# Kernel optimization log

Measured on AMD Instinct MI355X. Metric: run time of the kernel, lower is better.

Reference implementation:

```python
import jax, jax.numpy as jnp
import numpy as np

BS, L, D, H, NL, ITEM_NUM = 128, 64, 512, 8, 2, 100000
NEG_INF = -10000.0


def _ln(x):
    m = jnp.mean(x, axis=-1, keepdims=True)
    v = jnp.var(x, axis=-1, keepdims=True)
    return (x - m) * jax.lax.rsqrt(v + 1e-5)


def _user_encoder(input_embs, log_mask, pos_emb, qkv_w, out_w, ffn_w1, ffn_w2):
    # SASRec-style causal transformer encoder (post-LN blocks)
    B, S, d = input_embs.shape
    dh = d // H
    x = _ln(input_embs + pos_emb[None, :, :])
    pad = (log_mask != 0)                                  # [B,S]
    causal = jnp.tril(jnp.ones((S, S), dtype=bool))
    attn_ok = causal[None, :, :] & pad[:, None, :]         # [B,S,S]
    bias = jnp.where(attn_ok, 0.0, NEG_INF)[:, None, :, :]  # [B,1,S,S]
    for l in range(NL):
        qkv = x @ qkv_w[l]                                 # [B,S,3d]
        q, k, v = jnp.split(qkv, 3, axis=-1)
        q = q.reshape(B, S, H, dh).transpose(0, 2, 1, 3)
        k = k.reshape(B, S, H, dh).transpose(0, 2, 1, 3)
        v = v.reshape(B, S, H, dh).transpose(0, 2, 1, 3)
        scores = jnp.einsum('bhqd,bhkd->bhqk', q, k) / jnp.sqrt(jnp.asarray(dh, x.dtype)) + bias
        attn = jax.nn.softmax(scores, axis=-1)
        o = jnp.einsum('bhqk,bhkd->bhqd', attn, v).transpose(0, 2, 1, 3).reshape(B, S, d)
        x = _ln(x + o @ out_w[l])
        h = jax.nn.gelu(x @ ffn_w1[l])
        x = _ln(x + h @ ffn_w2[l])
    return x


def setup_inputs() -> dict:
    key = jax.random.key(0)
    ks = jax.random.split(key, 9)
    sample_items_id = jax.random.randint(ks[0], (BS, L + 1), 0, ITEM_NUM + 1)
    log_mask = jax.random.randint(ks[1], (BS, L), 0, 2).astype(jnp.float32)
    emb_table = (jax.random.normal(ks[2], (ITEM_NUM + 1, D), jnp.float32) * 0.02).at[0].set(0.0)
    pos_emb = jax.random.normal(ks[3], (L, D), jnp.float32) * 0.02
    qkv_w = jax.random.normal(ks[4], (NL, D, 3 * D), jnp.float32) * (D ** -0.5)
    out_w = jax.random.normal(ks[5], (NL, D, D), jnp.float32) * (D ** -0.5)
    ffn_w1 = jax.random.normal(ks[6], (NL, D, 4 * D), jnp.float32) * (D ** -0.5)
    ffn_w2 = jax.random.normal(ks[7], (NL, 4 * D, D), jnp.float32) * ((4 * D) ** -0.5)
    pop_prob = jax.random.uniform(ks[8], (ITEM_NUM + 1,), jnp.float32, 1e-6, 1.0)
    return dict(sample_items_id=sample_items_id, log_mask=log_mask, emb_table=emb_table,
                pos_emb=pos_emb, qkv_w=qkv_w, out_w=out_w, ffn_w1=ffn_w1, ffn_w2=ffn_w2,
                pop_prob=pop_prob)


def reference(sample_items_id, log_mask, emb_table, pos_emb, qkv_w, out_w, ffn_w1, ffn_w2, pop_prob):
    bs, l = log_mask.shape
    N = bs * (l + 1)
    items_flat = sample_items_id.reshape(-1)                        # [N]
    debias = jnp.log(pop_prob[items_flat])                          # [N]
    score_embs = emb_table[items_flat]                              # [N, D]
    input_embs = score_embs.reshape(bs, l + 1, -1)
    prec = _user_encoder(input_embs[:, :-1, :], log_mask, pos_emb, qkv_w, out_w, ffn_w1, ffn_w2)
    prec = prec.reshape(bs * l, -1)                                 # [bs*L, D]
    logits = prec @ score_embs.T - debias[None, :]                  # [bs*L, N]
    # padding-column mask (concat(log_mask, ones) == 0)
    pad_cols = jnp.concatenate([log_mask, jnp.ones((bs, 1), log_mask.dtype)], axis=1).reshape(-1) == 0
    logits = jnp.where(pad_cols[None, :], NEG_INF, logits)
    logits = logits.reshape(bs, l, N)
    # in-batch dedup mask: column k masked for batch i if item k appears in batch i's items
    id_list = sample_items_id.reshape(bs, l + 1)
    member = (items_flat[None, :, None] == id_list[:, None, :]).any(-1)   # [bs, N]
    target_col = jnp.arange(bs)[:, None] * (l + 1) + jnp.arange(1, l + 1)[None, :]  # [bs, L]
    is_target = jnp.arange(N)[None, None, :] == target_col[:, :, None]    # [bs, L, N]
    dedup = member[:, None, :] & ~is_target
    logits = jnp.where(dedup, NEG_INF, logits).reshape(bs * l, N)
    labels = target_col.reshape(-1)                                 # [bs*L]
    logp = jax.nn.log_softmax(logits, axis=-1)
    nll = -jnp.take_along_axis(logp, labels[:, None], axis=1)[:, 0]
    valid = (log_mask.reshape(-1) != 0).astype(logits.dtype)
    return (nll * valid).sum() / valid.sum()
```

## Files before the change

### kernel.cpp

```cpp
#include <hip/hip_runtime.h>
#include <hip/hip_bf16.h>
#include <cstdint>
#include <cstddef>

#define NEG_INF -10000.0f

constexpr int BSZ  = 128;
constexpr int SEQ  = 64;
constexpr int DIM  = 512;
constexpr int HEADS = 8;
constexpr int NLAYER = 2;
constexpr int NCOL = BSZ * (SEQ + 1);
constexpr int NCOLP = 8448;
constexpr int NROW = BSZ * SEQ;
constexpr int NSTRIP = NCOLP / 64;
constexpr float CMAX = 40.0f;

typedef __attribute__((ext_vector_type(8))) short bf16x8;
typedef __attribute__((ext_vector_type(4))) float f32x4;

__device__ __forceinline__ void async_copy16(const void* g, void* l) {
    __builtin_amdgcn_global_load_lds(
        (const __attribute__((address_space(1))) void*)g,
        (__attribute__((address_space(3))) void*)l, 16, 0, 0);
}

__device__ __forceinline__ float b2f(uint16_t u) {
    return __builtin_bit_cast(float, (uint32_t)u << 16);
}
__device__ __forceinline__ uint16_t f2b(float f) {
    __hip_bfloat16 h = __float2bfloat16(f);
    return __builtin_bit_cast(uint16_t, h);
}

__device__ __forceinline__ float gelu_f(float v) {
    float u = 0.7978845608028654f * (v + 0.044715f * v * v * v);
    return 0.5f * v * (1.0f + tanhf(u));
}

__device__ __forceinline__ void swizzle_rc(int id, int& ry, int& cx) {
    ry = (id & 7) * 8 + ((id >> 3) & 7);
    cx = id >> 6;
}

#define BAR() __builtin_amdgcn_s_barrier()
#define LGKM0() asm volatile("s_waitcnt lgkmcnt(0)" ::: "memory")
#define VMCNT(n) asm volatile("s_waitcnt vmcnt(" #n ")" ::: "memory")

__global__ __launch_bounds__(256) void gather_posln_kernel(
    const int* __restrict__ ids, const float* __restrict__ table,
    const float* __restrict__ pop, const float* __restrict__ pos,
    __hip_bfloat16* __restrict__ sebf, float* __restrict__ debias,
    __hip_bfloat16* __restrict__ xb) {
    const int w = threadIdx.x >> 6, lane = threadIdx.x & 63;
    const int k = blockIdx.x * 4 + w;
    const int b = k / 65, s = k - b * 65;
    const int id = ids[k];
    const float* src = table + (size_t)id * DIM + lane * 8;
    float4 u0 = *(const float4*)src;
    float4 u1 = *(const float4*)(src + 4);
    float v[8] = {u0.x, u0.y, u0.z, u0.w, u1.x, u1.y, u1.z, u1.w};
    bf16x8 se;
    #pragma unroll
    for (int j = 0; j < 8; j++) se[j] = (short)f2b(v[j]);
    *(bf16x8*)((uint16_t*)sebf + (size_t)k * DIM + lane * 8) = se;
    if (lane == 0) debias[k] = logf(pop[id]);
    if (s < 64) {
        const float* pp = pos + (size_t)s * DIM + lane * 8;
        float4 p0 = *(const float4*)pp;
        float4 p1 = *(const float4*)(pp + 4);
        float t[8] = {v[0] + p0.x, v[1] + p0.y, v[2] + p0.z, v[3] + p0.w,
                      v[4] + p1.x, v[5] + p1.y, v[6] + p1.z, v[7] + p1.w};
        float sum = 0.f, sq = 0.f;
        #pragma unroll
        for (int j = 0; j < 8; j++) { sum += t[j]; sq += t[j] * t[j]; }
        #pragma unroll
        for (int off = 32; off > 0; off >>= 1) {
            sum += __shfl_xor(sum, off, 64);
            sq  += __shfl_xor(sq,  off, 64);
        }
        const float mean = sum * (1.0f / 512.0f);
        const float var  = sq * (1.0f / 512.0f) - mean * mean;
        const float rs = rsqrtf(var + 1e-5f);
        bf16x8 o;
        #pragma unroll
        for (int j = 0; j < 8; j++) o[j] = (short)f2b((t[j] - mean) * rs);
        *(bf16x8*)((uint16_t*)xb + (size_t)(b * 64 + s) * DIM + lane * 8) = o;
    }
}

__global__ __launch_bounds__(256) void mask_kernel(
    const int* __restrict__ ids, const float* __restrict__ log_mask,
    uint8_t* __restrict__ colmask, uint8_t* __restrict__ padcol) {
    const int bi = blockIdx.x >> 3, seg = blockIdx.x & 7;
    __shared__ int sid[65];
    if (threadIdx.x < 65) sid[threadIdx.x] = ids[bi * 65 + threadIdx.x];
    __syncthreads();
    const int kend = (seg + 1) * (NCOLP / 8);
    for (int k = seg * (NCOLP / 8) + threadIdx.x; k < kend; k += 256) {
        uint8_t cmv, pcv;
        if (k < NCOL) {
            const int id = ids[k];
            bool mem = false;
            #pragma unroll
            for (int j = 0; j < 65; j++) mem |= (sid[j] == id);
            const int i2 = k / 65, jj = k - i2 * 65;
            const bool pc = (jj < 64) && (log_mask[i2 * 64 + jj] == 0.0f);
            cmv = (mem || pc) ? 1 : 0;
            pcv = pc ? 1 : 0;
        } else { cmv = 1; pcv = 1; }
        colmask[(size_t)bi * NCOLP + k] = cmv;
        if (bi == 0) padcol[k] = pcv;
    }
}

__global__ __launch_bounds__(256) void transpose_bf16_kernel(
    const float* __restrict__ W, __hip_bfloat16* __restrict__ WT, int K, int N) {
    __shared__ float tile[32][33];
    const size_t loff = (size_t)blockIdx.z * K * N;
    const int nt = blockIdx.x * 32, kt = blockIdx.y * 32;
    const int c = threadIdx.x & 31, r = threadIdx.x >> 5;
    #pragma unroll
    for (int p = 0; p < 4; p++)
        tile[p * 8 + r][c] = W[loff + (size_t)(kt + p * 8 + r) * N + nt + c];
    __syncthreads();
    #pragma unroll
    for (int p = 0; p < 4; p++)
        WT[loff + (size_t)(nt + p * 8 + r) * K + kt + c] = __float2bfloat16(tile[c][p * 8 + r]);
}

__global__ __launch_bounds__(256) void resid_ln_kernel(
    __hip_bfloat16* __restrict__ xb, const __hip_bfloat16* __restrict__ y) {
    const int w = threadIdx.x >> 6, lane = threadIdx.x & 63;
    const int row = blockIdx.x * 4 + w;
    uint16_t* xp = (uint16_t*)xb + (size_t)row * DIM + lane * 8;
    const uint16_t* yp = (const uint16_t*)y + (size_t)row * DIM + lane * 8;
    bf16x8 xv = *(const bf16x8*)xp;
    bf16x8 yv = *(const bf16x8*)yp;
    float t[8];
    float sum = 0.f, sq = 0.f;
    #pragma unroll
    for (int j = 0; j < 8; j++) {
        t[j] = b2f((uint16_t)xv[j]) + b2f((uint16_t)yv[j]);
        sum += t[j]; sq += t[j] * t[j];
    }
    #pragma unroll
    for (int off = 32; off > 0; off >>= 1) {
        sum += __shfl_xor(sum, off, 64);
        sq  += __shfl_xor(sq,  off, 64);
    }
    const float mean = sum * (1.0f / 512.0f);
    const float var  = sq * (1.0f / 512.0f) - mean * mean;
    const float rs = rsqrtf(var + 1e-5f);
    bf16x8 o;
    #pragma unroll
    for (int j = 0; j < 8; j++) o[j] = (short)f2b((t[j] - mean) * rs);
    *(bf16x8*)xp = o;
}

template<int TN, bool GELU>
__global__ __launch_bounds__(256) void gemm_bt_kernel(
    const __hip_bfloat16* __restrict__ A, const __hip_bfloat16* __restrict__ Bt,
    __hip_bfloat16* __restrict__ C, int N, int K) {
    __shared__ uint16_t As[2][128][32];
    __shared__ uint16_t Bs[2][TN][32];
    const int tid = threadIdx.x, w = tid >> 6, lane = tid & 63;
    const int quad = lane >> 4, l15 = lane & 15;
    constexpr int AI = (TN == 128) ? 4 : 2;
    const int wr = (TN == 128) ? (w >> 1) : w;
    const int wc = (TN == 128) ? (w & 1) : 0;
    const int rowbase = wr * (AI * 16);
    int ry, cx;
    swizzle_rc(blockIdx.x, ry, cx);
    const int row0 = ry * 128, col0 = cx * TN;
    const uint16_t* Ag = (const uint16_t*)A;
    const uint16_t* Bg = (const uint16_t*)Bt;
    const int sr = lane >> 2, sc = (lane & 3) * 8;
    f32x4 acc[AI][4];
    #pragma unroll
    for (int i = 0; i < AI; i++)
        #pragma unroll
        for (int j = 0; j < 4; j++) acc[i][j] = {0.f, 0.f, 0.f, 0.f};

    for (int k0 = 0; k0 < K; k0 += 64) {
        #pragma unroll
        for (int h = 0; h < 2; h++) {
            #pragma unroll
            for (int i = 0; i < 2; i++) {
                const int rb = w * 32 + i * 16;
                async_copy16(Ag + (size_t)(row0 + rb + sr) * K + k0 + h * 32 + sc, &As[h][rb][0]);
            }
            if (TN == 128) {
                #pragma unroll
                for (int i = 0; i < 2; i++) {
                    const int rb = w * 32 + i * 16;
                    async_copy16(Bg + (size_t)(col0 + rb + sr) * K + k0 + h * 32 + sc, &Bs[h][rb][0]);
                }
            } else {
                const int rb = w * 16;
                async_copy16(Bg + (size_t)(col0 + rb + sr) * K + k0 + h * 32 + sc, &Bs[h][rb][0]);
            }
        }
        __syncthreads();
        #pragma unroll
        for (int h = 0; h < 2; h++) {
            bf16x8 af[AI], bfr[4];
            #pragma unroll
            for (int i = 0; i < AI; i++)
                af[i] = *(const bf16x8*)&As[h][rowbase + i * 16 + l15][quad * 8];
            #pragma unroll
            for (int j = 0; j < 4; j++)
                bfr[j] = *(const bf16x8*)&Bs[h][wc * 64 + j * 16 + l15][quad * 8];
            #pragma unroll
            for (int i = 0; i < AI; i++)
                #pragma unroll
                for (int j = 0; j < 4; j++)
                    acc[i][j] = __builtin_amdgcn_mfma_f32_16x16x32_bf16(af[i], bfr[j], acc[i][j], 0, 0, 0);
        }
        __syncthreads();
    }
    #pragma unroll
    for (int i = 0; i < AI; i++) {
        #pragma unroll
        for (int r = 0; r < 4; r++) {
            const int row = row0 + rowbase + i * 16 + quad * 4 + r;
            #pragma unroll
            for (int j = 0; j < 4; j++) {
                const int col = col0 + wc * 64 + j * 16 + l15;
                float v = acc[i][j][r];
                if (GELU) v = gelu_f(v);
                C[(size_t)row * N + col] = __float2bfloat16(v);
            }
        }
    }
}

__global__ __launch_bounds__(256) void attn_mfma_kernel(
    const __hip_bfloat16* __restrict__ qkv, const float* __restrict__ log_mask,
    __hip_bfloat16* __restrict__ obuf) {
    constexpr int QS = 72;
    constexpr int VS32 = 36;
    __shared__ uint16_t Qs[64 * QS];
    __shared__ uint16_t Ks_[64 * QS];
    __shared__ uint16_t Ps[64 * QS];
    __shared__ uint32_t Vt32[64 * VS32];
    __shared__ float mask_s[64];
    const int b = blockIdx.x >> 3, h = blockIdx.x & 7;
    const int tid = threadIdx.x, w = tid >> 6, lane = tid & 63;
    const int quad = lane >> 4, l15 = lane & 15;
    const uint16_t* qg = (const uint16_t*)qkv;

    if (tid < 64) mask_s[tid] = log_mask[b * 64 + tid];
    #pragma unroll
    for (int it = 0; it < 2; it++) {
        const int idx = it * 256 + tid;
        const int s = idx >> 3, c = (idx & 7) * 8;
        const size_t gbase = (size_t)(b * 64 + s) * 1536 + h * 64 + c;
        *(bf16x8*)&Qs[s * QS + c]  = *(const bf16x8*)&qg[gbase];
        *(bf16x8*)&Ks_[s * QS + c] = *(const bf16x8*)&qg[gbase + 512];
    }
    {
        const int sp = tid >> 3;
        const int c = (tid & 7) * 8;
        const size_t gbase = (size_t)(b * 64 + sp * 2) * 1536 + 1024 + h * 64 + c;
        bf16x8 v0 = *(const bf16x8*)&qg[gbase];
        bf16x8 v1 = *(const bf16x8*)&qg[gbase + 1536];
        #pragma unroll
        for (int jj = 0; jj < 8; jj++)
            Vt32[(c + jj) * VS32 + sp] =
                (uint32_t)(uint16_t)v0[jj] | ((uint32_t)(uint16_t)v1[jj] << 16);
    }
    __syncthreads();

    f32x4 sacc[4];
    #pragma unroll
    for (int j = 0; j < 4; j++) sacc[j] = {0.f, 0.f, 0.f, 0.f};
    #pragma unroll
    for (int k0 = 0; k0 < 2; k0++) {
        bf16x8 aq = *(const bf16x8*)&Qs[(w * 16 + l15) * QS + k0 * 32 + quad * 8];
        #pragma unroll
        for (int j = 0; j < 4; j++) {
            bf16x8 bk = *(const bf16x8*)&Ks_[(j * 16 + l15) * QS + k0 * 32 + quad * 8];
            sacc[j] = __builtin_amdgcn_mfma_f32_16x16x32_bf16(aq, bk, sacc[j], 0, 0, 0);
        }
    }
    #pragma unroll
    for (int r = 0; r < 4; r++) {
        const int q = w * 16 + quad * 4 + r;
        float vals[4];
        float vmax = -3.0e38f;
        #pragma unroll
        for (int j = 0; j < 4; j++) {
            const int col = j * 16 + l15;
            const bool ok = (col <= q) && (mask_s[col] != 0.0f);
            float v = sacc[j][r] * 0.125f + (ok ? 0.0f : NEG_INF);
            vals[j] = v;
            vmax = fmaxf(vmax, v);
        }
        #pragma unroll
        for (int off = 1; off < 16; off <<= 1) vmax = fmaxf(vmax, __shfl_xor(vmax, off, 64));
        float e[4], s = 0.f;
        #pragma unroll
        for (int j = 0; j < 4; j++) { e[j] = __expf(vals[j] - vmax); s += e[j]; }
        #pragma unroll
        for (int off = 1; off < 16; off <<= 1) s += __shfl_xor(s, off, 64);
        const float inv = 1.0f / s;
        #pragma unroll
        for (int j = 0; j < 4; j++)
            Ps[q * QS + j * 16 + l15] = f2b(e[j] * inv);
    }
    __syncthreads();

    f32x4 oacc[4];
    #pragma unroll
    for (int j = 0; j < 4; j++) oacc[j] = {0.f, 0.f, 0.f, 0.f};
    #pragma unroll
    for (int k0 = 0; k0 < 2; k0++) {
        bf16x8 ap = *(const bf16x8*)&Ps[(w * 16 + l15) * QS + k0 * 32 + quad * 8];
        #pragma unroll
        for (int j = 0; j < 4; j++) {
            bf16x8 bv = *(const bf16x8*)&Vt32[(j * 16 + l15) * VS32 + k0 * 16 + quad * 4];
            oacc[j] = __builtin_amdgcn_mfma_f32_16x16x32_bf16(ap, bv, oacc[j], 0, 0, 0);
        }
    }
    #pragma unroll
    for (int r = 0; r < 4; r++) {
        const int q = w * 16 + quad * 4 + r;
        #pragma unroll
        for (int j = 0; j < 4; j++) {
            const int d = j * 16 + l15;
            obuf[(size_t)(b * 64 + q) * 512 + h * 64 + d] = __float2bfloat16(oacc[j][r]);
        }
    }
}

template<int EPI>
__global__ __launch_bounds__(512) void gemm256_kernel(
    const __hip_bfloat16* __restrict__ A, const __hip_bfloat16* __restrict__ Bt,
    __hip_bfloat16* __restrict__ C, int N, int K,
    const float* __restrict__ debias, const uint8_t* __restrict__ colmask,
    float* __restrict__ partials) {
    __shared__ uint16_t SA[2][2][128 * 64];
    __shared__ uint16_t SB[2][2][128 * 64];
    __shared__ float dc_s[256];
    __shared__ uint8_t cm_s[4][256];

    const int tid = threadIdx.x;
    const int w = tid >> 6, lane = tid & 63;
    const int quad = lane >> 4, l15 = lane & 15;
    const int wr = w >> 2, wc = w & 3;

    const int kb = blockIdx.x >> 3;
    const int ry = (blockIdx.x & 7) * 4 + (kb & 3), cx = kb >> 2;
    const int row0 = ry * 256, col0 = cx * 256;

    const uint16_t* Ag = (const uint16_t*)A;
    const uint16_t* Bg = (const uint16_t*)Bt;

    if (EPI == 2) {
        if (tid < 256) dc_s[tid] = debias[col0 + tid] + CMAX;
        #pragma unroll
        for (int j = 0; j < 2; j++) {
            const int e = j * 512 + tid;
            cm_s[e >> 8][e & 255] =
                colmask[(size_t)((row0 >> 6) + (e >> 8)) * NCOLP + col0 + (e & 255)];
        }
    }

    const int tb0 = w << 6, tb1 = 512 + (w << 6);
    const uint16_t* gA[2][2];
    const uint16_t* gB[2][2];
    #pragma unroll
    for (int j = 0; j < 2; j++) {
        const int t = j * 512 + (w << 6) + lane;
        const int r = t >> 3;
        const int s = (t & 7) ^ (r & 7);
        #pragma unroll
        for (int h = 0; h < 2; h++) {
            gA[h][j] = Ag + (size_t)(row0 + h * 128 + r) * K + s * 8;
            gB[h][j] = Bg + (size_t)(col0 + h * 128 + r) * K + s * 8;
        }
    }

    #define STAGE_A(tile, half, k0) do { \
        async_copy16(gA[half][0] + (k0), &SA[tile][half][tb0 * 8]); \
        async_copy16(gA[half][1] + (k0), &SA[tile][half][tb1 * 8]); } while (0)
    #define STAGE_B(tile, half, k0) do { \
        async_copy16(gB[half][0] + (k0), &SB[tile][half][tb0 * 8]); \
        async_copy16(gB[half][1] + (k0), &SB[tile][half][tb1 * 8]); } while (0)

    auto fragA = [&](int tile, int m, int kk) -> bf16x8 {
        return *(const bf16x8*)&SA[tile][wr]
            [((m * 16 + l15) << 6) + ((((kk << 2) + quad) ^ (l15 & 7)) << 3)];
    };
    auto fragB = [&](int tile, int n, int kk) -> bf16x8 {
        return *(const bf16x8*)&SB[tile][wc >> 1]
            [(((wc & 1) * 64 + n * 16 + l15) << 6) + ((((kk << 2) + quad) ^ (l15 & 7)) << 3)];
    };

    f32x4 acc[8][4];
    #pragma unroll
    for (int m = 0; m < 8; m++)
        #pragma unroll
        for (int n = 0; n < 4; n++) acc[m][n] = {0.f, 0.f, 0.f, 0.f};

    STAGE_A(0, 0, 0); STAGE_A(0, 1, 0);
    STAGE_B(0, 0, 0); STAGE_B(0, 1, 0);
    STAGE_A(1, 0, 64); STAGE_B(1, 0, 64);
    VMCNT(4);
    BAR();

    const int niters = K >> 7;
    bf16x8 af[4][2], bA[2][2], bB[2][2];
    for (int it = 0; it < niters; ++it) {
        const bool st = (it + 1 < niters);
        const int kc = it << 7;
        const int kn = kc + 128;

        #pragma unroll
        for (int m = 0; m < 4; m++) { af[m][0] = fragA(0, m, 0); af[m][1] = fragA(0, m, 1); }
        #pragma unroll
        for (int n = 0; n < 2; n++) { bA[n][0] = fragB(0, n, 0); bA[n][1] = fragB(0, n, 1); }
        STAGE_A(1, 1, kc + 64);
        BAR(); LGKM0();
        __builtin_amdgcn_s_setprio(1);
        #pragma unroll
        for (int m = 0; m < 4; m++)
            #pragma unroll
            for (int n = 0; n < 2; n++) {
                acc[m][n] = __builtin_amdgcn_mfma_f32_16x16x32_bf16(af[m][0], bA[n][0], acc[m][n], 0, 0, 0);
                acc[m][n] = __builtin_amdgcn_mfma_f32_16x16x32_bf16(af[m][1], bA[n][1], acc[m][n], 0, 0, 0);
            }
        __builtin_amdgcn_s_setprio(0);
        BAR();

        #pragma unroll
        for (int n = 0; n < 2; n++) { bB[n][0] = fragB(0, n + 2, 0); bB[n][1] = fragB(0, n + 2, 1); }
        STAGE_B(1, 1, kc + 64);
        BAR(); LGKM0();
        __builtin_amdgcn_s_setprio(1);
        #pragma unroll
        for (int m = 0; m < 4; m++)
            #pragma unroll
            for (int n = 0; n < 2; n++) {
                acc[m][n + 2] = __builtin_amdgcn_mfma_f32_16x16x32_bf16(af[m][0], bB[n][0], acc[m][n + 2], 0, 0, 0);
                acc[m][n + 2] = __builtin_amdgcn_mfma_f32_16x16x32_bf16(af[m][1], bB[n][1], acc[m][n + 2], 0, 0, 0);
            }
        __builtin_amdgcn_s_setprio(0);
        BAR();

        #pragma unroll
        for (int m = 0; m < 4; m++) { af[m][0] = fragA(0, m + 4, 0); af[m][1] = fragA(0, m + 4, 1); }
        if (st) STAGE_B(0, 0, kn);
        BAR(); LGKM0();
        __builtin_amdgcn_s_setprio(1);
        #pragma unroll
        for (int m = 0; m < 4; m++)
            #pragma unroll
            for (int n = 0; n < 2; n++) {
                acc[m + 4][n + 2] = __builtin_amdgcn_mfma_f32_16x16x32_bf16(af[m][0], bB[n][0], acc[m + 4][n + 2], 0, 0, 0);
                acc[m + 4][n + 2] = __builtin_amdgcn_mfma_f32_16x16x32_bf16(af[m][1], bB[n][1], acc[m + 4][n + 2], 0, 0, 0);
            }
        __builtin_amdgcn_s_setprio(0);
        BAR();

        if (st) STAGE_A(0, 0, kn);
        __builtin_amdgcn_s_setprio(1);
        #pragma unroll
        for (int m = 0; m < 4; m++)
            #pragma unroll
            for (int n = 0; n < 2; n++) {
                acc[m + 4][n] = __builtin_amdgcn_mfma_f32_16x16x32_bf16(af[m][0], bA[n][0], acc[m + 4][n], 0, 0, 0);
                acc[m + 4][n] = __builtin_amdgcn_mfma_f32_16x16x32_bf16(af[m][1], bA[n][1], acc[m + 4][n], 0, 0, 0);
            }
        __builtin_amdgcn_s_setprio(0);
        if (st) { VMCNT(4); } else { VMCNT(0); }
        BAR();

        #pragma unroll
        for (int m = 0; m < 4; m++) { af[m][0] = fragA(1, m, 0); af[m][1] = fragA(1, m, 1); }
        #pragma unroll
        for (int n = 0; n < 2; n++) { bA[n][0] = fragB(1, n, 0); bA[n][1] = fragB(1, n, 1); }
        if (st) STAGE_A(0, 1, kn);
        BAR(); LGKM0();
        __builtin_amdgcn_s_setprio(1);
        #pragma unroll
        for (int m = 0; m < 4; m++)
            #pragma unroll
            for (int n = 0; n < 2; n++) {
                acc[m][n] = __builtin_amdgcn_mfma_f32_16x16x32_bf16(af[m][0], bA[n][0], acc[m][n], 0, 0, 0);
                acc[m][n] = __builtin_amdgcn_mfma_f32_16x16x32_bf16(af[m][1], bA[n][1], acc[m][n], 0, 0, 0);
            }
        __builtin_amdgcn_s_setprio(0);
        BAR();

        #pragma unroll
        for (int n = 0; n < 2; n++) { bB[n][0] = fragB(1, n + 2, 0); bB[n][1] = fragB(1, n + 2, 1); }
        if (st) STAGE_B(0, 1, kn);
        BAR(); LGKM0();
        __builtin_amdgcn_s_setprio(1);
        #pragma unroll
        for (int m = 0; m < 4; m++)
            #pragma unroll
            for (int n = 0; n < 2; n++) {
                acc[m][n + 2] = __builtin_amdgcn_mfma_f32_16x16x32_bf16(af[m][0], bB[n][0], acc[m][n + 2], 0, 0, 0);
                acc[m][n + 2] = __builtin_amdgcn_mfma_f32_16x16x32_bf16(af[m][1], bB[n][1], acc[m][n + 2], 0, 0, 0);
            }
        __builtin_amdgcn_s_setprio(0);
        BAR();

        #pragma unroll
        for (int m = 0; m < 4; m++) { af[m][0] = fragA(1, m + 4, 0); af[m][1] = fragA(1, m + 4, 1); }
        if (st) STAGE_B(1, 0, kn + 64);
        BAR(); LGKM0();
        __builtin_amdgcn_s_setprio(1);
        #pragma unroll
        for (int m = 0; m < 4; m++)
            #pragma unroll
            for (int n = 0; n < 2; n++) {
                acc[m + 4][n + 2] = __builtin_amdgcn_mfma_f32_16x16x32_bf16(af[m][0], bB[n][0], acc[m + 4][n + 2], 0, 0, 0);
                acc[m + 4][n + 2] = __builtin_amdgcn_mfma_f32_16x16x32_bf16(af[m][1], bB[n][1], acc[m + 4][n + 2], 0, 0, 0);
            }
        __builtin_amdgcn_s_setprio(0);
        BAR();

        if (st) STAGE_A(1, 0, kn + 64);
        __builtin_amdgcn_s_setprio(1);
        #pragma unroll
        for (int m = 0; m < 4; m++)
            #pragma unroll
            for (int n = 0; n < 2; n++) {
                acc[m + 4][n] = __builtin_amdgcn_mfma_f32_16x16x32_bf16(af[m][0], bA[n][0], acc[m + 4][n], 0, 0, 0);
                acc[m + 4][n] = __builtin_amdgcn_mfma_f32_16x16x32_bf16(af[m][1], bA[n][1], acc[m + 4][n], 0, 0, 0);
            }
        __builtin_amdgcn_s_setprio(0);
        if (st) { VMCNT(4); BAR(); }
    }

    if (EPI == 2) {
        const int strip = cx * 4 + wc;
        #pragma unroll
        for (int m = 0; m < 8; m++) {
            #pragma unroll
            for (int r = 0; r < 4; r++) {
                const int lrow = wr * 128 + m * 16 + quad * 4 + r;
                const int row = row0 + lrow;
                float s = 0.f;
                #pragma unroll
                for (int n = 0; n < 4; n++) {
                    const int lcol = wc * 64 + n * 16 + l15;
                    float t = acc[m][n][r] - dc_s[lcol];
                    t = (cm_s[lrow >> 6][lcol] != 0) ? -1.0e30f : t;
                    s += __expf(t);
                }
                #pragma unroll
                for (int off = 1; off < 16; off <<= 1) s += __shfl_xor(s, off, 64);
                if (l15 == 0) partials[(size_t)row * NSTRIP + strip] = s;
            }
        }
    } else {
        #pragma unroll
        for (int m = 0; m < 8; m++) {
            #pragma unroll
            for (int r = 0; r < 4; r++) {
                const int row = row0 + wr * 128 + m * 16 + quad * 4 + r;
                #pragma unroll
                for (int n = 0; n < 4; n++) {
                    const int col = col0 + wc * 64 + n * 16 + l15;
                    float v = acc[m][n][r];
                    if (EPI == 1) v = gelu_f(v);
                    C[(size_t)row * N + col] = __float2bfloat16(v);
                }
            }
        }
    }
    #undef STAGE_A
    #undef STAGE_B
}

__global__ __launch_bounds__(256) void label_kernel(
    const __hip_bfloat16* __restrict__ xb, const __hip_bfloat16* __restrict__ sebf,
    const float* __restrict__ debias, const uint8_t* __restrict__ padcol,
    float* __restrict__ lab) {
    const int w = threadIdx.x >> 6, lane = threadIdx.x & 63;
    const int row = blockIdx.x * 4 + w;
    const int b = row >> 6, s0 = row & 63;
    const int k = b * 65 + s0 + 1;
    const uint16_t* xp = (const uint16_t*)xb + (size_t)row * DIM + lane * 8;
    const uint16_t* sp = (const uint16_t*)sebf + (size_t)k * DIM + lane * 8;
    bf16x8 xv = *(const bf16x8*)xp;
    bf16x8 sv = *(const bf16x8*)sp;
    float a = 0.f;
    #pragma unroll
    for (int j = 0; j < 8; j++) a += b2f((uint16_t)xv[j]) * b2f((uint16_t)sv[j]);
    #pragma unroll
    for (int off = 32; off > 0; off >>= 1) a += __shfl_xor(a, off, 64);
    if (lane == 0)
        lab[row] = padcol[k] ? NEG_INF : (a - debias[k]);
}

__global__ __launch_bounds__(256) void combine_kernel(
    const float* __restrict__ partials, const float* __restrict__ label_logit,
    const float* __restrict__ log_mask, float* __restrict__ bsums) {
    const int row = blockIdx.x * 256 + threadIdx.x;
    const float lab = label_logit[row];
    float Ls = __expf(lab - CMAX);
    const float4* pr = (const float4*)(partials + (size_t)row * NSTRIP);
    for (int t = 0; t < NSTRIP / 4; t++) {
        float4 v = pr[t];
        Ls += v.x + v.y + v.z + v.w;
    }
    const float lse = CMAX + logf(Ls);
    const float valid = (log_mask[row] != 0.0f) ? 1.0f : 0.0f;
    float a = (lse - lab) * valid;
    float c = valid;
    __shared__ float sa[4], sc_[4];
    #pragma unroll
    for (int off = 32; off > 0; off >>= 1) {
        a += __shfl_down(a, off, 64);
        c += __shfl_down(c, off, 64);
    }
    const int lane = threadIdx.x & 63, w = threadIdx.x >> 6;
    if (lane == 0) { sa[w] = a; sc_[w] = c; }
    __syncthreads();
    if (threadIdx.x == 0) {
        bsums[blockIdx.x * 2 + 0] = sa[0] + sa[1] + sa[2] + sa[3];
        bsums[blockIdx.x * 2 + 1] = sc_[0] + sc_[1] + sc_[2] + sc_[3];
    }
}

__global__ __launch_bounds__(64) void finalize_kernel(
    const float* __restrict__ bsums, float* __restrict__ out) {
    const int t = threadIdx.x;
    float a = 0.f, c = 0.f;
    if (t < 32) { a = bsums[2 * t]; c = bsums[2 * t + 1]; }
    #pragma unroll
    for (int off = 32; off > 0; off >>= 1) {
        a += __shfl_down(a, off, 64);
        c += __shfl_down(c, off, 64);
    }
    if (t == 0) out[0] = a / c;
}

extern "C" void kernel_launch(void* const* d_in, const int* in_sizes, int n_in,
                              void* d_out, int out_size, void* d_ws, size_t ws_size,
                              hipStream_t stream) {
    const int*   ids    = (const int*)d_in[0];
    const float* lm     = (const float*)d_in[1];
    const float* emb    = (const float*)d_in[2];
    const float* pos    = (const float*)d_in[3];
    const float* qkv_w  = (const float*)d_in[4];
    const float* out_w  = (const float*)d_in[5];
    const float* ffn1_w = (const float*)d_in[6];
    const float* ffn2_w = (const float*)d_in[7];
    const float* pop    = (const float*)d_in[8];
    float* out = (float*)d_out;

    char* p = (char*)d_ws;
    auto alloc = [&](size_t bytes) {
        char* r = p;
        p += (bytes + 255) & ~(size_t)255;
        return r;
    };
    typedef __hip_bfloat16 bf16;
    bf16*    sebf     = (bf16*)alloc((size_t)NCOLP * DIM * 2);
    float*   debias   = (float*)alloc((size_t)NCOLP * 4);
    uint8_t* padcol   = (uint8_t*)alloc(NCOLP);
    uint8_t* colmask  = (uint8_t*)alloc((size_t)BSZ * NCOLP);
    bf16*    xb       = (bf16*)alloc((size_t)NROW * DIM * 2);
    bf16*    big      = (bf16*)alloc((size_t)NROW * 2048 * 2);
    bf16*    tmp1     = (bf16*)alloc((size_t)NROW * DIM * 2);
    bf16*    tmp2     = (bf16*)alloc((size_t)NROW * DIM * 2);
    float*   partials = (float*)alloc((size_t)NROW * NSTRIP * 4);
    float*   lab      = (float*)alloc((size_t)NROW * 4);
    float*   bsums    = (float*)alloc(64 * 4);
    bf16*    qkvT     = (bf16*)alloc((size_t)NLAYER * 1536 * 512 * 2);
    bf16*    outT     = (bf16*)alloc((size_t)NLAYER * 512 * 512 * 2);
    bf16*    f1T      = (bf16*)alloc((size_t)NLAYER * 2048 * 512 * 2);
    bf16*    f2T      = (bf16*)alloc((size_t)NLAYER * 512 * 2048 * 2);

    transpose_bf16_kernel<<<dim3(1536 / 32, 512 / 32, NLAYER), 256, 0, stream>>>(
        qkv_w, qkvT, 512, 1536);
    transpose_bf16_kernel<<<dim3(512 / 32, 512 / 32, NLAYER), 256, 0, stream>>>(
        out_w, outT, 512, 512);
    transpose_bf16_kernel<<<dim3(2048 / 32, 512 / 32, NLAYER), 256, 0, stream>>>(
        ffn1_w, f1T, 512, 2048);
    transpose_bf16_kernel<<<dim3(512 / 32, 2048 / 32, NLAYER), 256, 0, stream>>>(
        ffn2_w, f2T, 2048, 512);

    gather_posln_kernel<<<NCOL / 4, 256, 0, stream>>>(ids, emb, pop, pos, sebf, debias, xb);
    mask_kernel<<<BSZ * 8, 256, 0, stream>>>(ids, lm, colmask, padcol);

    for (int l = 0; l < NLAYER; l++) {
        gemm256_kernel<0><<<32 * (1536 / 256), 512, 0, stream>>>(
            xb, qkvT + (size_t)l * 1536 * 512, big, 1536, 512, nullptr, nullptr, nullptr);
        attn_mfma_kernel<<<BSZ * HEADS, 256, 0, stream>>>(big, lm, tmp1);
        gemm_bt_kernel<64, false><<<(512 / 64) * 64, 256, 0, stream>>>(
            tmp1, outT + (size_t)l * 512 * 512, tmp2, 512, 512);
        resid_ln_kernel<<<NROW / 4, 256, 0, stream>>>(xb, tmp2);
        gemm256_kernel<1><<<32 * (2048 / 256), 512, 0, stream>>>(
            xb, f1T + (size_t)l * 2048 * 512, big, 2048, 512, nullptr, nullptr, nullptr);
        gemm_bt_kernel<64, false><<<(512 / 64) * 64, 256, 0, stream>>>(
            big, f2T + (size_t)l * 512 * 2048, tmp2, 512, 2048);
        resid_ln_kernel<<<NROW / 4, 256, 0, stream>>>(xb, tmp2);
    }

    label_kernel<<<NROW / 4, 256, 0, stream>>>(xb, sebf, debias, padcol, lab);
    gemm256_kernel<2><<<32 * (NCOLP / 256), 512, 0, stream>>>(
        xb, sebf, nullptr, NCOLP, 512, debias, colmask, partials);
    combine_kernel<<<NROW / 256, 256, 0, stream>>>(partials, lab, lm, bsums);
    finalize_kernel<<<1, 64, 0, stream>>>(bsums, out);
}
```

Measured before the change: 727.8 us.

## Make logits GEMM persistent with cross-tile prefetch; use smaller GEMM for QKV/FFN1

The logits GEMM becomes a persistent kernel with 256 blocks, each walking a contiguous range of 256x256 tiles. The first k-slices of the next tile are prefetched during the last k-iteration of the current one, so tile-boundary load latency is hidden and the wave-quantization tail is removed. Debias and column-mask values are now read straight from global memory in the epilogue instead of being staged in shared memory. The QKV and FFN1 projections switch from the 256-tile kernel to the existing 128-wide gemm_bt_kernel, which launches more, smaller blocks and may reuse data less per block.

Result: faster. 671.9 us (-7.7%).

```diff
diff --git a/kernel.cpp b/kernel.cpp
--- a/kernel.cpp
+++ b/kernel.cpp
@@ -334,245 +334,243 @@
     }
 }
 
-template<int EPI>
-__global__ __launch_bounds__(512) void gemm256_kernel(
+__global__ __launch_bounds__(512) void logits256_kernel(
     const __hip_bfloat16* __restrict__ A, const __hip_bfloat16* __restrict__ Bt,
-    __hip_bfloat16* __restrict__ C, int N, int K,
     const float* __restrict__ debias, const uint8_t* __restrict__ colmask,
     float* __restrict__ partials) {
+    constexpr int K = 512;
+    constexpr int NC = NCOLP / 256;
+    constexpr int TPX = 4 * NC;
+    constexpr int NITER = K >> 7;
     __shared__ uint16_t SA[2][2][128 * 64];
     __shared__ uint16_t SB[2][2][128 * 64];
-    __shared__ float dc_s[256];
-    __shared__ uint8_t cm_s[4][256];
 
     const int tid = threadIdx.x;
     const int w = tid >> 6, lane = tid & 63;
     const int quad = lane >> 4, l15 = lane & 15;
     const int wr = w >> 2, wc = w & 3;
 
-    const int kb = blockIdx.x >> 3;
-    const int ry = (blockIdx.x & 7) * 4 + (kb & 3), cx = kb >> 2;
-    const int row0 = ry * 256, col0 = cx * 256;
+    const int x = blockIdx.x & 7, sub = blockIdx.x >> 3;
+    int lam = (sub * TPX) >> 5;
+    const int lamE = ((sub + 1) * TPX) >> 5;
+    if (lam >= lamE) return;
 
     const uint16_t* Ag = (const uint16_t*)A;
     const uint16_t* Bg = (const uint16_t*)Bt;
 
-    if (EPI == 2) {
-        if (tid < 256) dc_s[tid] = debias[col0 + tid] + CMAX;
-        #pragma unroll
-        for (int j = 0; j < 2; j++) {
-            const int e = j * 512 + tid;
-            cm_s[e >> 8][e & 255] =
-                colmask[(size_t)((row0 >> 6) + (e >> 8)) * NCOLP + col0 + (e & 255)];
-        }
-    }
-
-    const int tb0 = w << 6, tb1 = 512 + (w << 6);
-    const uint16_t* gA[2][2];
-    const uint16_t* gB[2][2];
+    int offS[2][2];
     #pragma unroll
     for (int j = 0; j < 2; j++) {
         const int t = j * 512 + (w << 6) + lane;
         const int r = t >> 3;
         const int s = (t & 7) ^ (r & 7);
         #pragma unroll
-        for (int h = 0; h < 2; h++) {
-            gA[h][j] = Ag + (size_t)(row0 + h * 128 + r) * K + s * 8;
-            gB[h][j] = Bg + (size_t)(col0 + h * 128 + r) * K + s * 8;
-        }
-    }
-
-    #define STAGE_A(tile, half, k0) do { \
-        async_copy16(gA[half][0] + (k0), &SA[tile][half][tb0 * 8]); \
-        async_copy16(gA[half][1] + (k0), &SA[tile][half][tb1 * 8]); } while (0)
-    #define STAGE_B(tile, half, k0) do { \
-        async_copy16(gB[half][0] + (k0), &SB[tile][half][tb0 * 8]); \
-        async_copy16(gB[half][1] + (k0), &SB[tile][half][tb1 * 8]); } while (0)
-
-    auto fragA = [&](int tile, int m, int kk) -> bf16x8 {
-        return *(const bf16x8*)&SA[tile][wr]
+        for (int h = 0; h < 2; h++) offS[h][j] = (h * 128 + r) * K + s * 8;
+    }
+    const int db0 = (w << 6) * 8, db1 = 4096 + (w << 6) * 8;
+
+    #define STAGE_A(slot, half, base, k0) do { \
+        async_copy16(Ag + (base) + offS[half][0] + (k0), &SA[slot][half][db0]); \
+        async_copy16(Ag + (base) + offS[half][1] + (k0), &SA[slot][half][db1]); } while (0)
+    #define STAGE_B(slot, half, base, k0) do { \
+        async_copy16(Bg + (base) + offS[half][0] + (k0), &SB[slot][half][db0]); \
+        async_copy16(Bg + (base) + offS[half][1] + (k0), &SB[slot][half][db1]); } while (0)
+
+    auto fragA = [&](int slot, int m, int kk) -> bf16x8 {
+        return *(const bf16x8*)&SA[slot][wr]
             [((m * 16 + l15) << 6) + ((((kk << 2) + quad) ^ (l15 & 7)) << 3)];
     };
-    auto fragB = [&](int tile, int n, int kk) -> bf16x8 {
-        return *(const bf16x8*)&SB[tile][wc >> 1]
+    auto fragB = [&](int slot, int n, int kk) -> bf16x8 {
+        return *(const bf16x8*)&SB[slot][wc >> 1]
             [(((wc & 1) * 64 + n * 16 + l15) << 6) + ((((kk << 2) + quad) ^ (l15 & 7)) << 3)];
     };
 
+    int ry = x * 4 + lam / NC, cx = lam % NC;
+    size_t baseA = (size_t)(ry * 256) * K;
+    size_t baseB = (size_t)(cx * 256) * K;
+
     f32x4 acc[8][4];
     #pragma unroll
     for (int m = 0; m < 8; m++)
         #pragma unroll
         for (int n = 0; n < 4; n++) acc[m][n] = {0.f, 0.f, 0.f, 0.f};
 
-    STAGE_A(0, 0, 0); STAGE_A(0, 1, 0);
-    STAGE_B(0, 0, 0); STAGE_B(0, 1, 0);
-    STAGE_A(1, 0, 64); STAGE_B(1, 0, 64);
+    STAGE_A(0, 0, baseA, 0); STAGE_A(0, 1, baseA, 0);
+    STAGE_B(0, 0, baseB, 0); STAGE_B(0, 1, baseB, 0);
+    STAGE_A(1, 0, baseA, 64); STAGE_B(1, 0, baseB, 64);
     VMCNT(4);
     BAR();
 
-    const int niters = K >> 7;
     bf16x8 af[4][2], bA[2][2], bB[2][2];
-    for (int it = 0; it < niters; ++it) {
-        const bool st = (it + 1 < niters);
-        const int kc = it << 7;
-        const int kn = kc + 128;
-
-        #pragma unroll
-        for (int m = 0; m < 4; m++) { af[m][0] = fragA(0, m, 0); af[m][1] = fragA(0, m, 1); }
-        #pragma unroll
-        for (int n = 0; n < 2; n++) { bA[n][0] = fragB(0, n, 0); bA[n][1] = fragB(0, n, 1); }
-        STAGE_A(1, 1, kc + 64);
-        BAR(); LGKM0();
-        __builtin_amdgcn_s_setprio(1);
-        #pragma unroll
-        for (int m = 0; m < 4; m++)
-            #pragma unroll
-            for (int n = 0; n < 2; n++) {
-                acc[m][n] = __builtin_amdgcn_mfma_f32_16x16x32_bf16(af[m][0], bA[n][0], acc[m][n], 0, 0, 0);
-                acc[m][n] = __builtin_amdgcn_mfma_f32_16x16x32_bf16(af[m][1], bA[n][1], acc[m][n], 0, 0, 0);
+    for (; lam < lamE; ++lam) {
+        const bool hasNext = (lam + 1 < lamE);
+        int ryn = 0, cxn = 0;
+        size_t baseAn = 0, baseBn = 0;
+        if (hasNext) {
+            ryn = x * 4 + (lam + 1) / NC; cxn = (lam + 1) % NC;
+            baseAn = (size_t)(ryn * 256) * K;
+            baseBn = (size_t)(cxn * 256) * K;
+        }
+        for (int it = 0; it < NITER; ++it) {
+            const bool lastIt = (it == NITER - 1);
+            const bool stC = !lastIt;
+            const bool stX = lastIt && hasNext;
+            const int kc = it << 7, kn = kc + 128;
+
+            #pragma unroll
+            for (int m = 0; m < 4; m++) { af[m][0] = fragA(0, m, 0); af[m][1] = fragA(0, m, 1); }
+            #pragma unroll
+            for (int n = 0; n < 2; n++) { bA[n][0] = fragB(0, n, 0); bA[n][1] = fragB(0, n, 1); }
+            STAGE_A(1, 1, baseA, kc + 64);
+            BAR(); LGKM0();
+            __builtin_amdgcn_s_setprio(1);
+            #pragma unroll
+            for (int m = 0; m < 4; m++)
+                #pragma unroll
+                for (int n = 0; n < 2; n++) {
+                    acc[m][n] = __builtin_amdgcn_mfma_f32_16x16x32_bf16(af[m][0], bA[n][0], acc[m][n], 0, 0, 0);
+                    acc[m][n] = __builtin_amdgcn_mfma_f32_16x16x32_bf16(af[m][1], bA[n][1], acc[m][n], 0, 0, 0);
+                }
+            __builtin_amdgcn_s_setprio(0);
+            BAR();
+
+            #pragma unroll
+            for (int n = 0; n < 2; n++) { bB[n][0] = fragB(0, n + 2, 0); bB[n][1] = fragB(0, n + 2, 1); }
+            STAGE_B(1, 1, baseB, kc + 64);
+            BAR(); LGKM0();
+            __builtin_amdgcn_s_setprio(1);
+            #pragma unroll
+            for (int m = 0; m < 4; m++)
+                #pragma unroll
+                for (int n = 0; n < 2; n++) {
+                    acc[m][n + 2] = __builtin_amdgcn_mfma_f32_16x16x32_bf16(af[m][0], bB[n][0], acc[m][n + 2], 0, 0, 0);
+                    acc[m][n + 2] = __builtin_amdgcn_mfma_f32_16x16x32_bf16(af[m][1], bB[n][1], acc[m][n + 2], 0, 0, 0);
+                }
+            __builtin_amdgcn_s_setprio(0);
+            BAR();
+
+            #pragma unroll
+            for (int m = 0; m < 4; m++) { af[m][0] = fragA(0, m + 4, 0); af[m][1] = fragA(0, m + 4, 1); }
+            if (stC) STAGE_B(0, 0, baseB, kn); else if (stX) STAGE_B(0, 0, baseBn, 0);
+            BAR(); LGKM0();
+            __builtin_amdgcn_s_setprio(1);
+            #pragma unroll
+            for (int m = 0; m < 4; m++)
+                #pragma unroll
+                for (int n = 0; n < 2; n++) {
+                    acc[m + 4][n + 2] = __builtin_amdgcn_mfma_f32_16x16x32_bf16(af[m][0], bB[n][0], acc[m + 4][n + 2], 0, 0, 0);
+                    acc[m + 4][n + 2] = __builtin_amdgcn_mfma_f32_16x16x32_bf16(af[m][1], bB[n][1], acc[m + 4][n + 2], 0, 0, 0);
+                }
+            __builtin_amdgcn_s_setprio(0);
+            BAR();
+
+            if (stC) STAGE_A(0, 0, baseA, kn); else if (stX) STAGE_A(0, 0, baseAn, 0);
+            __builtin_amdgcn_s_setprio(1);
+            #pragma unroll
+            for (int m = 0; m < 4; m++)
+                #pragma unroll
+                for (int n = 0; n < 2; n++) {
+                    acc[m + 4][n] = __builtin_amdgcn_mfma_f32_16x16x32_bf16(af[m][0], bA[n][0], acc[m + 4][n], 0, 0, 0);
+                    acc[m + 4][n] = __builtin_amdgcn_mfma_f32_16x16x32_bf16(af[m][1], bA[n][1], acc[m + 4][n], 0, 0, 0);
+                }
+            __builtin_amdgcn_s_setprio(0);
+            if (stC || stX) { VMCNT(4); } else { VMCNT(0); }
+            BAR();
+
+            #pragma unroll
+            for (int m = 0; m < 4; m++) { af[m][0] = fragA(1, m, 0); af[m][1] = fragA(1, m, 1); }
+            #pragma unroll
+            for (int n = 0; n < 2; n++) { bA[n][0] = fragB(1, n, 0); bA[n][1] = fragB(1, n, 1); }
+            if (stC) STAGE_A(0, 1, baseA, kn); else if (stX) STAGE_A(0, 1, baseAn, 0);
+            BAR(); LGKM0();
+            __builtin_amdgcn_s_setprio(1);
+            #pragma unroll
+            for (int m = 0; m < 4; m++)
+                #pragma unroll
+                for (int n = 0; n < 2; n++) {
+                    acc[m][n] = __builtin_amdgcn_mfma_f32_16x16x32_bf16(af[m][0], bA[n][0], acc[m][n], 0, 0, 0);
+                    acc[m][n] = __builtin_amdgcn_mfma_f32_16x16x32_bf16(af[m][1], bA[n][1], acc[m][n], 0, 0, 0);
+                }
+            __builtin_amdgcn_s_setprio(0);
+            BAR();
+
+            #pragma unroll
+            for (int n = 0; n < 2; n++) { bB[n][0] = fragB(1, n + 2, 0); bB[n][1] = fragB(1, n + 2, 1); }
+            if (stC) STAGE_B(0, 1, baseB, kn); else if (stX) STAGE_B(0, 1, baseBn, 0);
+            BAR(); LGKM0();
+            __builtin_amdgcn_s_setprio(1);
+            #pragma unroll
+            for (int m = 0; m < 4; m++)
+                #pragma unroll
+                for (int n = 0; n < 2; n++) {
+                    acc[m][n + 2] = __builtin_amdgcn_mfma_f32_16x16x32_bf16(af[m][0], bB[n][0], acc[m][n + 2], 0, 0, 0);
+                    acc[m][n + 2] = __builtin_amdgcn_mfma_f32_16x16x32_bf16(af[m][1], bB[n][1], acc[m][n + 2], 0, 0, 0);
+                }
+            __builtin_amdgcn_s_setprio(0);
+            BAR();
+
+            #pragma unroll
+            for (int m = 0; m < 4; m++) { af[m][0] = fragA(1, m + 4, 0); af[m][1] = fragA(1, m + 4, 1); }
+            if (stC) STAGE_B(1, 0, baseB, kn + 64); else if (stX) STAGE_B(1, 0, baseBn, 64);
+            BAR(); LGKM0();
+            __builtin_amdgcn_s_setprio(1);
+            #pragma unroll
+            for (int m = 0; m < 4; m++)
+                #pragma unroll
+                for (int n = 0; n < 2; n++) {
+                    acc[m + 4][n + 2] = __builtin_amdgcn_mfma_f32_16x16x32_bf16(af[m][0], bB[n][0], acc[m + 4][n + 2], 0, 0, 0);
+                    acc[m + 4][n + 2] = __builtin_amdgcn_mfma_f32_16x16x32_bf16(af[m][1], bB[n][1], acc[m + 4][n + 2], 0, 0, 0);
+                }
+            __builtin_amdgcn_s_setprio(0);
+            BAR();
+
+            if (stC) STAGE_A(1, 0, baseA, kn + 64); else if (stX) STAGE_A(1, 0, baseAn, 64);
+            __builtin_amdgcn_s_setprio(1);
+            #pragma unroll
+            for (int m = 0; m < 4; m++)
+                #pragma unroll
+                for (int n = 0; n < 2; n++) {
+                    acc[m + 4][n] = __builtin_amdgcn_mfma_f32_16x16x32_bf16(af[m][0], bA[n][0], acc[m + 4][n], 0, 0, 0);
+                    acc[m + 4][n] = __builtin_amdgcn_mfma_f32_16x16x32_bf16(af[m][1], bA[n][1], acc[m + 4][n], 0, 0, 0);
+                }
+            __builtin_amdgcn_s_setprio(0);
+            if (stC || stX) { VMCNT(4); BAR(); }
+        }
+
+        {
+            const int strip = cx * 4 + wc;
+            const int col0 = cx * 256;
+            float deb[4]; uint8_t cmv[2][4];
+            #pragma unroll
+            for (int n = 0; n < 4; n++) {
+                const int lcol = wc * 64 + n * 16 + l15;
+                deb[n] = debias[col0 + lcol] + CMAX;
+                cmv[0][n] = colmask[(size_t)(ry * 4 + wr * 2 + 0) * NCOLP + col0 + lcol];
+                cmv[1][n] = colmask[(size_t)(ry * 4 + wr * 2 + 1) * NCOLP + col0 + lcol];
             }
-        __builtin_amdgcn_s_setprio(0);
-        BAR();
-
-        #pragma unroll
-        for (int n = 0; n < 2; n++) { bB[n][0] = fragB(0, n + 2, 0); bB[n][1] = fragB(0, n + 2, 1); }
-        STAGE_B(1, 1, kc + 64);
-        BAR(); LGKM0();
-        __builtin_amdgcn_s_setprio(1);
-        #pragma unroll
-        for (int m = 0; m < 4; m++)
-            #pragma unroll
-            for (int n = 0; n < 2; n++) {
-                acc[m][n + 2] = __builtin_amdgcn_mfma_f32_16x16x32_bf16(af[m][0], bB[n][0], acc[m][n + 2], 0, 0, 0);
-                acc[m][n + 2] = __builtin_amdgcn_mfma_f32_16x16x32_bf16(af[m][1], bB[n][1], acc[m][n + 2], 0, 0, 0);
+            #pragma unroll
+            for (int m = 0; m < 8; m++) {
+                #pragma unroll
+                for (int r = 0; r < 4; r++) {
+                    const int row = ry * 256 + wr * 128 + m * 16 + quad * 4 + r;
+                    float s = 0.f;
+                    #pragma unroll
+                    for (int n = 0; n < 4; n++) {
+                        float t = acc[m][n][r] - deb[n];
+                        t = (cmv[m >> 2][n] != 0) ? -1.0e30f : t;
+                        s += __expf(t);
+                    }
+                    #pragma unroll
+                    for (int off = 1; off < 16; off <<= 1) s += __shfl_xor(s, off, 64);
+                    if (l15 == 0) partials[(size_t)row * NSTRIP + strip] = s;
+                }
             }
-        __builtin_amdgcn_s_setprio(0);
-        BAR();
-
-        #pragma unroll
-        for (int m = 0; m < 4; m++) { af[m][0] = fragA(0, m + 4, 0); af[m][1] = fragA(0, m + 4, 1); }
-        if (st) STAGE_B(0, 0, kn);
-        BAR(); LGKM0();
-        __builtin_amdgcn_s_setprio(1);
-        #pragma unroll
-        for (int m = 0; m < 4; m++)
-            #pragma unroll
-            for (int n = 0; n < 2; n++) {
-                acc[m + 4][n + 2] = __builtin_amdgcn_mfma_f32_16x16x32_bf16(af[m][0], bB[n][0], acc[m + 4][n + 2], 0, 0, 0);
-                acc[m + 4][n + 2] = __builtin_amdgcn_mfma_f32_16x16x32_bf16(af[m][1], bB[n][1], acc[m + 4][n + 2], 0, 0, 0);
-            }
-        __builtin_amdgcn_s_setprio(0);
-        BAR();
-
-        if (st) STAGE_A(0, 0, kn);
-        __builtin_amdgcn_s_setprio(1);
-        #pragma unroll
-        for (int m = 0; m < 4; m++)
-            #pragma unroll
-            for (int n = 0; n < 2; n++) {
-                acc[m + 4][n] = __builtin_amdgcn_mfma_f32_16x16x32_bf16(af[m][0], bA[n][0], acc[m + 4][n], 0, 0, 0);
-                acc[m + 4][n] = __builtin_amdgcn_mfma_f32_16x16x32_bf16(af[m][1], bA[n][1], acc[m + 4][n], 0, 0, 0);
-            }
-        __builtin_amdgcn_s_setprio(0);
-        if (st) { VMCNT(4); } else { VMCNT(0); }
-        BAR();
-
-        #pragma unroll
-        for (int m = 0; m < 4; m++) { af[m][0] = fragA(1, m, 0); af[m][1] = fragA(1, m, 1); }
-        #pragma unroll
-        for (int n = 0; n < 2; n++) { bA[n][0] = fragB(1, n, 0); bA[n][1] = fragB(1, n, 1); }
-        if (st) STAGE_A(0, 1, kn);
-        BAR(); LGKM0();
-        __builtin_amdgcn_s_setprio(1);
-        #pragma unroll
-        for (int m = 0; m < 4; m++)
-            #pragma unroll
-            for (int n = 0; n < 2; n++) {
-                acc[m][n] = __builtin_amdgcn_mfma_f32_16x16x32_bf16(af[m][0], bA[n][0], acc[m][n], 0, 0, 0);
-                acc[m][n] = __builtin_amdgcn_mfma_f32_16x16x32_bf16(af[m][1], bA[n][1], acc[m][n], 0, 0, 0);
-            }
-        __builtin_amdgcn_s_setprio(0);
-        BAR();
-
-        #pragma unroll
-        for (int n = 0; n < 2; n++) { bB[n][0] = fragB(1, n + 2, 0); bB[n][1] = fragB(1, n + 2, 1); }
-        if (st) STAGE_B(0, 1, kn);
-        BAR(); LGKM0();
-        __builtin_amdgcn_s_setprio(1);
-        #pragma unroll
-        for (int m = 0; m < 4; m++)
-            #pragma unroll
-            for (int n = 0; n < 2; n++) {
-                acc[m][n + 2] = __builtin_amdgcn_mfma_f32_16x16x32_bf16(af[m][0], bB[n][0], acc[m][n + 2], 0, 0, 0);
-                acc[m][n + 2] = __builtin_amdgcn_mfma_f32_16x16x32_bf16(af[m][1], bB[n][1], acc[m][n + 2], 0, 0, 0);
-            }
-        __builtin_amdgcn_s_setprio(0);
-        BAR();
-
-        #pragma unroll
-        for (int m = 0; m < 4; m++) { af[m][0] = fragA(1, m + 4, 0); af[m][1] = fragA(1, m + 4, 1); }
-        if (st) STAGE_B(1, 0, kn + 64);
-        BAR(); LGKM0();
-        __builtin_amdgcn_s_setprio(1);
-        #pragma unroll
-        for (int m = 0; m < 4; m++)
-            #pragma unroll
-            for (int n = 0; n < 2; n++) {
-                acc[m + 4][n + 2] = __builtin_amdgcn_mfma_f32_16x16x32_bf16(af[m][0], bB[n][0], acc[m + 4][n + 2], 0, 0, 0);
-                acc[m + 4][n + 2] = __builtin_amdgcn_mfma_f32_16x16x32_bf16(af[m][1], bB[n][1], acc[m + 4][n + 2], 0, 0, 0);
-            }
-        __builtin_amdgcn_s_setprio(0);
-        BAR();
-
-        if (st) STAGE_A(1, 0, kn + 64);
-        __builtin_amdgcn_s_setprio(1);
-        #pragma unroll
-        for (int m = 0; m < 4; m++)
-            #pragma unroll
-            for (int n = 0; n < 2; n++) {
-                acc[m + 4][n] = __builtin_amdgcn_mfma_f32_16x16x32_bf16(af[m][0], bA[n][0], acc[m + 4][n], 0, 0, 0);
-                acc[m + 4][n] = __builtin_amdgcn_mfma_f32_16x16x32_bf16(af[m][1], bA[n][1], acc[m + 4][n], 0, 0, 0);
-            }
-        __builtin_amdgcn_s_setprio(0);
-        if (st) { VMCNT(4); BAR(); }
-    }
-
-    if (EPI == 2) {
-        const int strip = cx * 4 + wc;
-        #pragma unroll
-        for (int m = 0; m < 8; m++) {
-            #pragma unroll
-            for (int r = 0; r < 4; r++) {
-                const int lrow = wr * 128 + m * 16 + quad * 4 + r;
-                const int row = row0 + lrow;
-                float s = 0.f;
-                #pragma unroll
-                for (int n = 0; n < 4; n++) {
-                    const int lcol = wc * 64 + n * 16 + l15;
-                    float t = acc[m][n][r] - dc_s[lcol];
-                    t = (cm_s[lrow >> 6][lcol] != 0) ? -1.0e30f : t;
-                    s += __expf(t);
-                }
-                #pragma unroll
-                for (int off = 1; off < 16; off <<= 1) s += __shfl_xor(s, off, 64);
-                if (l15 == 0) partials[(size_t)row * NSTRIP + strip] = s;
-            }
-        }
-    } else {
-        #pragma unroll
-        for (int m = 0; m < 8; m++) {
-            #pragma unroll
-            for (int r = 0; r < 4; r++) {
-                const int row = row0 + wr * 128 + m * 16 + quad * 4 + r;
-                #pragma unroll
-                for (int n = 0; n < 4; n++) {
-                    const int col = col0 + wc * 64 + n * 16 + l15;
-                    float v = acc[m][n][r];
-                    if (EPI == 1) v = gelu_f(v);
-                    C[(size_t)row * N + col] = __float2bfloat16(v);
-                }
-            }
-        }
+            #pragma unroll
+            for (int m = 0; m < 8; m++)
+                #pragma unroll
+                for (int n = 0; n < 4; n++) acc[m][n] = {0.f, 0.f, 0.f, 0.f};
+        }
+        ry = ryn; cx = cxn; baseA = baseAn; baseB = baseBn;
     }
     #undef STAGE_A
     #undef STAGE_B
@@ -692,22 +690,21 @@
     mask_kernel<<<BSZ * 8, 256, 0, stream>>>(ids, lm, colmask, padcol);
 
     for (int l = 0; l < NLAYER; l++) {
-        gemm256_kernel<0><<<32 * (1536 / 256), 512, 0, stream>>>(
-            xb, qkvT + (size_t)l * 1536 * 512, big, 1536, 512, nullptr, nullptr, nullptr);
+        gemm_bt_kernel<128, false><<<(1536 / 128) * 64, 256, 0, stream>>>(
+            xb, qkvT + (size_t)l * 1536 * 512, big, 1536, 512);
         attn_mfma_kernel<<<BSZ * HEADS, 256, 0, stream>>>(big, lm, tmp1);
         gemm_bt_kernel<64, false><<<(512 / 64) * 64, 256, 0, stream>>>(
             tmp1, outT + (size_t)l * 512 * 512, tmp2, 512, 512);
         resid_ln_kernel<<<NROW / 4, 256, 0, stream>>>(xb, tmp2);
-        gemm256_kernel<1><<<32 * (2048 / 256), 512, 0, stream>>>(
-            xb, f1T + (size_t)l * 2048 * 512, big, 2048, 512, nullptr, nullptr, nullptr);
+        gemm_bt_kernel<128, true><<<(2048 / 128) * 64, 256, 0, stream>>>(
+            xb, f1T + (size_t)l * 2048 * 512, big, 2048, 512);
         gemm_bt_kernel<64, false><<<(512 / 64) * 64, 256, 0, stream>>>(
             big, f2T + (size_t)l * 512 * 2048, tmp2, 512, 2048);
         resid_ln_kernel<<<NROW / 4, 256, 0, stream>>>(xb, tmp2);
     }
 
     label_kernel<<<NROW / 4, 256, 0, stream>>>(xb, sebf, debias, padcol, lab);
-    gemm256_kernel<2><<<32 * (NCOLP / 256), 512, 0, stream>>>(
-        xb, sebf, nullptr, NCOLP, 512, debias, colmask, partials);
+    logits256_kernel<<<256, 512, 0, stream>>>(xb, sebf, debias, colmask, partials);
     combine_kernel<<<NROW / 256, 256, 0, stream>>>(partials, lab, lm, bsums);
     finalize_kernel<<<1, 64, 0, stream>>>(bsums, out);
 }
```
